# Kernel optimization log

Hardware: AMD Instinct MI355X
Metric: run time of the kernel (lower is better)

The kernel has to match this reference:

```python
import jax, jax.numpy as jnp
import numpy as np

N_RAYS = 262144  # 512x512 image
N_PTS = 64       # hardcoded in original forward (reshape(-1, 64, 3))
FAR_DELTA = 1e10 # sentinel delta appended for the last sample


def setup_inputs() -> dict:
    key = jax.random.key(0)
    k1, k2, k3 = jax.random.split(key, 3)
    # non-negative densities, as a density field would produce
    density = jax.random.uniform(k1, (N_RAYS, N_PTS, 1), dtype=jnp.float32)
    # sorted depths along each ray in [2, 6] (typical near/far bounds)
    depth_values = jnp.sort(
        2.0 + 4.0 * jax.random.uniform(k2, (N_RAYS, N_PTS), dtype=jnp.float32),
        axis=-1,
    )
    rays_feature = jax.random.uniform(k3, (N_RAYS, N_PTS, 3), dtype=jnp.float32)
    return {"density": density, "depth_values": depth_values, "rays_feature": rays_feature}


def reference(density, depth_values, rays_feature):
    # deltas: consecutive depth differences, with huge sentinel for last sample
    deltas = jnp.concatenate(
        [depth_values[:, 1:] - depth_values[:, :-1],
         jnp.full_like(depth_values[:, :1], FAR_DELTA)],
        axis=-1,
    )  # (N, P)
    sigma_delta = density[..., 0] * deltas          # (N, P)
    trans_step = jnp.exp(-sigma_delta)              # per-segment transmittance e
    # exclusive cumulative product: T_0 = 1, T_i = prod_{j<i} e_j
    transmittance = jnp.concatenate(
        [jnp.ones_like(trans_step[:, :1]),
         jnp.cumprod(trans_step[:, :-1], axis=1)],
        axis=1,
    )  # (N, P)
    weights = transmittance * (1.0 - trans_step)    # (N, P)
    feature = jnp.sum(weights[..., None] * rays_feature, axis=1)  # (N, 3)
    depth = jnp.sum(weights * depth_values, axis=1)               # (N,)
    return feature, depth
```

## Files before the change

kernel.cpp:

```cpp
#include <hip/hip_runtime.h>

#define N_RAYS 262144
#define N_PTS  64
#define FAR_DELTA 1e10f
#define RAYS_PER_BLOCK 16

__global__ __launch_bounds__(256) void volume_render_kernel(
    const float* __restrict__ density,
    const float* __restrict__ depth_values,
    const float* __restrict__ rays_feature,
    float* __restrict__ out)
{
    const int lane = threadIdx.x & 63;
    const int wave = threadIdx.x >> 6;
    const int sub  = lane >> 4;
    const int l    = lane & 15;
    const int ray  = blockIdx.x * RAYS_PER_BLOCK + wave * 4 + sub;

    const float4 d  = ((const float4*)depth_values)[(long)ray * 16 + l];
    const float4 sg = ((const float4*)density)[(long)ray * 16 + l];

    const float4* fp = (const float4*)rays_feature + (long)ray * 48 + l * 3;
    const float4 fa = fp[0];
    const float4 fb = fp[1];
    const float4 fc = fp[2];

    const float dnx = __shfl_down(d.x, 1, 16);
    const float dl0 = d.y - d.x;
    const float dl1 = d.z - d.y;
    const float dl2 = d.w - d.z;
    const float dl3 = (l == 15) ? FAR_DELTA : (dnx - d.w);

    const float e0 = __expf(-sg.x * dl0);
    const float e1 = __expf(-sg.y * dl1);
    const float e2 = __expf(-sg.z * dl2);
    const float e3 = __expf(-sg.w * dl3);

    const float q1 = e0;
    const float q2 = q1 * e1;
    const float q3 = q2 * e2;

    float ptot = q3 * e3;
    #pragma unroll
    for (int off = 1; off < 16; off <<= 1) {
        float t = __shfl_up(ptot, off, 16);
        if (l >= off) ptot *= t;
    }
    float p_exc = __shfl_up(ptot, 1, 16);
    if (l == 0) p_exc = 1.0f;

    const float w0 = p_exc *      (1.0f - e0);
    const float w1 = p_exc * q1 * (1.0f - e1);
    const float w2 = p_exc * q2 * (1.0f - e2);
    const float w3 = p_exc * q3 * (1.0f - e3);

    float fx = w0*fa.x + w1*fa.w + w2*fb.z + w3*fc.y;
    float fy = w0*fa.y + w1*fb.x + w2*fb.w + w3*fc.z;
    float fz = w0*fa.z + w1*fb.y + w2*fc.x + w3*fc.w;
    float wd = w0*d.x  + w1*d.y  + w2*d.z  + w3*d.w;

    #pragma unroll
    for (int off = 8; off > 0; off >>= 1) {
        fx += __shfl_xor(fx, off, 16);
        fy += __shfl_xor(fy, off, 16);
        fz += __shfl_xor(fz, off, 16);
        wd += __shfl_xor(wd, off, 16);
    }

    if (l < 3) {
        const float v = (l == 0) ? fx : ((l == 1) ? fy : fz);
        out[(long)ray * 3 + l] = v;
    } else if (l == 3) {
        out[(long)N_RAYS * 3 + ray] = wd;
    }
}

extern "C" void kernel_launch(void* const* d_in, const int* in_sizes, int n_in,
                              void* d_out, int out_size, void* d_ws, size_t ws_size,
                              hipStream_t stream) {
    const float* density      = (const float*)d_in[0];
    const float* depth_values = (const float*)d_in[1];
    const float* rays_feature = (const float*)d_in[2];
    float* out = (float*)d_out;

    const int blocks = N_RAYS / RAYS_PER_BLOCK;
    volume_render_kernel<<<blocks, 256, 0, stream>>>(
        density, depth_values, rays_feature, out);
}
```

Before: 351.2 us.

## Use persistent grid-stride waves with register prefetch of next ray group

Replaces the one-block-per-16-rays launch with a fixed grid of 2048 blocks. Each wave loops over several groups of four rays and prefetches the next group's depth, density and feature vectors into registers while it computes the current group. The aim is to hide global memory latency and cut block launch overhead in this bandwidth-bound kernel. In exchange, register pressure roughly doubles for the loaded data, which can lower occupancy, and the fixed grid size may not saturate all CUs.

New measurement: 356.9 us. Within noise of the previous version (+1.6%).

```diff
diff --git a/kernel.cpp b/kernel.cpp
--- a/kernel.cpp
+++ b/kernel.cpp
@@ -3,9 +3,13 @@
 #define N_RAYS 262144
 #define N_PTS  64
 #define FAR_DELTA 1e10f
-#define RAYS_PER_BLOCK 16
 
-__global__ __launch_bounds__(256) void volume_render_kernel(
+#define THREADS 256
+#define BLOCKS  2048
+#define NWAVES  (BLOCKS * (THREADS / 64))
+#define ITERS   (N_RAYS / (NWAVES * 4))
+
+__global__ __launch_bounds__(THREADS) void volume_render_kernel(
     const float* __restrict__ density,
     const float* __restrict__ depth_values,
     const float* __restrict__ rays_feature,
@@ -15,63 +19,80 @@
     const int wave = threadIdx.x >> 6;
     const int sub  = lane >> 4;
     const int l    = lane & 15;
-    const int ray  = blockIdx.x * RAYS_PER_BLOCK + wave * 4 + sub;
+    const int gw   = blockIdx.x * (THREADS / 64) + wave;
 
-    const float4 d  = ((const float4*)depth_values)[(long)ray * 16 + l];
-    const float4 sg = ((const float4*)density)[(long)ray * 16 + l];
+    float4 d, sg, fa, fb, fc;
 
-    const float4* fp = (const float4*)rays_feature + (long)ray * 48 + l * 3;
-    const float4 fa = fp[0];
-    const float4 fb = fp[1];
-    const float4 fc = fp[2];
-
-    const float dnx = __shfl_down(d.x, 1, 16);
-    const float dl0 = d.y - d.x;
-    const float dl1 = d.z - d.y;
-    const float dl2 = d.w - d.z;
-    const float dl3 = (l == 15) ? FAR_DELTA : (dnx - d.w);
-
-    const float e0 = __expf(-sg.x * dl0);
-    const float e1 = __expf(-sg.y * dl1);
-    const float e2 = __expf(-sg.z * dl2);
-    const float e3 = __expf(-sg.w * dl3);
-
-    const float q1 = e0;
-    const float q2 = q1 * e1;
-    const float q3 = q2 * e2;
-
-    float ptot = q3 * e3;
-    #pragma unroll
-    for (int off = 1; off < 16; off <<= 1) {
-        float t = __shfl_up(ptot, off, 16);
-        if (l >= off) ptot *= t;
-    }
-    float p_exc = __shfl_up(ptot, 1, 16);
-    if (l == 0) p_exc = 1.0f;
-
-    const float w0 = p_exc *      (1.0f - e0);
-    const float w1 = p_exc * q1 * (1.0f - e1);
-    const float w2 = p_exc * q2 * (1.0f - e2);
-    const float w3 = p_exc * q3 * (1.0f - e3);
-
-    float fx = w0*fa.x + w1*fa.w + w2*fb.z + w3*fc.y;
-    float fy = w0*fa.y + w1*fb.x + w2*fb.w + w3*fc.z;
-    float fz = w0*fa.z + w1*fb.y + w2*fc.x + w3*fc.w;
-    float wd = w0*d.x  + w1*d.y  + w2*d.z  + w3*d.w;
-
-    #pragma unroll
-    for (int off = 8; off > 0; off >>= 1) {
-        fx += __shfl_xor(fx, off, 16);
-        fy += __shfl_xor(fy, off, 16);
-        fz += __shfl_xor(fz, off, 16);
-        wd += __shfl_xor(wd, off, 16);
+    long ray = (long)gw * 4 + sub;
+    {
+        d  = ((const float4*)depth_values)[ray * 16 + l];
+        sg = ((const float4*)density)[ray * 16 + l];
+        const float4* fp = (const float4*)rays_feature + ray * 48 + l * 3;
+        fa = fp[0]; fb = fp[1]; fc = fp[2];
     }
 
-    if (l < 3) {
-        const float v = (l == 0) ? fx : ((l == 1) ? fy : fz);
-        out[(long)ray * 3 + l] = v;
-    } else if (l == 3) {
-        out[(long)N_RAYS * 3 + ray] = wd;
+    #pragma unroll 1
+    for (int it = 0; it < ITERS; ++it) {
+        const long nray = ray + (long)NWAVES * 4;
+        float4 nd, nsg, nfa, nfb, nfc;
+        if (it + 1 < ITERS) {
+            nd  = ((const float4*)depth_values)[nray * 16 + l];
+            nsg = ((const float4*)density)[nray * 16 + l];
+            const float4* nfp = (const float4*)rays_feature + nray * 48 + l * 3;
+            nfa = nfp[0]; nfb = nfp[1]; nfc = nfp[2];
+        }
+
+        const float dnx = __shfl_down(d.x, 1, 16);
+        const float dl0 = d.y - d.x;
+        const float dl1 = d.z - d.y;
+        const float dl2 = d.w - d.z;
+        const float dl3 = (l == 15) ? FAR_DELTA : (dnx - d.w);
+
+        const float e0 = __expf(-sg.x * dl0);
+        const float e1 = __expf(-sg.y * dl1);
+        const float e2 = __expf(-sg.z * dl2);
+        const float e3 = __expf(-sg.w * dl3);
+
+        const float q1 = e0;
+        const float q2 = q1 * e1;
+        const float q3 = q2 * e2;
+
+        float ptot = q3 * e3;
+        #pragma unroll
+        for (int off = 1; off < 16; off <<= 1) {
+            float t = __shfl_up(ptot, off, 16);
+            if (l >= off) ptot *= t;
+        }
+        float p_exc = __shfl_up(ptot, 1, 16);
+        if (l == 0) p_exc = 1.0f;
+
+        const float w0 = p_exc *      (1.0f - e0);
+        const float w1 = p_exc * q1 * (1.0f - e1);
+        const float w2 = p_exc * q2 * (1.0f - e2);
+        const float w3 = p_exc * q3 * (1.0f - e3);
+
+        float fx = w0*fa.x + w1*fa.w + w2*fb.z + w3*fc.y;
+        float fy = w0*fa.y + w1*fb.x + w2*fb.w + w3*fc.z;
+        float fz = w0*fa.z + w1*fb.y + w2*fc.x + w3*fc.w;
+        float wd = w0*d.x  + w1*d.y  + w2*d.z  + w3*d.w;
+
+        #pragma unroll
+        for (int off = 8; off > 0; off >>= 1) {
+            fx += __shfl_xor(fx, off, 16);
+            fy += __shfl_xor(fy, off, 16);
+            fz += __shfl_xor(fz, off, 16);
+            wd += __shfl_xor(wd, off, 16);
+        }
+
+        if (l < 3) {
+            const float v = (l == 0) ? fx : ((l == 1) ? fy : fz);
+            out[ray * 3 + l] = v;
+        } else if (l == 3) {
+            out[(long)N_RAYS * 3 + ray] = wd;
+        }
+
+        d = nd; sg = nsg; fa = nfa; fb = nfb; fc = nfc;
+        ray = nray;
     }
 }
 
@@ -83,7 +104,6 @@
     const float* rays_feature = (const float*)d_in[2];
     float* out = (float*)d_out;
 
-    const int blocks = N_RAYS / RAYS_PER_BLOCK;
-    volume_render_kernel<<<blocks, 256, 0, stream>>>(
+    volume_render_kernel<<<BLOCKS, THREADS, 0, stream>>>(
         density, depth_values, rays_feature, out);
 }
```
